# Performance work log

Measured on AMD Instinct MI355X. Metric: run time of the kernel, lower is better.

## Reference

```python
import jax, jax.numpy as jnp
import numpy as np

EMB = 300; TOWERS = 6; LAYERS = 4; EPS = 1e-5; F_OUT = EMB // TOWERS  # 50
N_NODES = 3000; N_EDGES = 9000; N_GRAPHS = 64
NODE_VOCAB = 16; EDGE_VOCAB = 4


def _bn(x, g, b, m, v):
    # eval-mode BatchNorm1d with running stats
    return (x - m) * jax.lax.rsqrt(v + EPS) * g + b


def _forward(node_emb, edge_emb, W_edge, b_edge, W_pre, b_pre, W_post, b_post,
             W_lin, b_lin, bn_gamma, bn_beta, bn_mean, bn_var,
             head_w0, head_b0, gn0_gamma, gn0_beta, gn0_mean, gn0_var,
             head_w1, head_b1, gn1_gamma, gn1_beta, gn1_mean, gn1_var,
             head_w2, head_b2, x, edge_index, edge_attr, batch, num_graphs):
    N = x.shape[0]
    src, dst = edge_index[0], edge_index[1]
    h = node_emb[x]            # [N, D] node encoder (categorical embedding)
    e = edge_emb[edge_attr]    # [E, D] edge encoder
    cnt = jax.ops.segment_sum(jnp.ones(src.shape, h.dtype), dst, num_segments=N)
    deg = jnp.maximum(cnt, 1.0)
    log_deg = jnp.log(deg + 1.0)
    avg_log = jnp.mean(jnp.log(cnt + 1.0))  # PNA avg_deg['log'] of degree histogram
    amp = (log_deg / avg_log)[:, None, None]
    att = (avg_log / log_deg)[:, None, None]
    has_nb = (cnt > 0)[:, None, None]
    degc = deg[:, None, None]

    h_list = [h]
    for l in range(LAYERS):
        eproj = e @ W_edge[l] + b_edge[l]                        # [E, D]
        hcat = jnp.concatenate([h[dst], h[src], eproj], -1)      # [E, 3D] = [x_i, x_j, e]
        m = jnp.einsum('ef,tfd->etd', hcat, W_pre[l]) + b_pre[l]  # [E, T, D] per-tower pre-MLP
        s = jax.ops.segment_sum(m, dst, num_segments=N)
        mean = s / degc
        mn = jnp.where(has_nb, jax.ops.segment_min(m, dst, num_segments=N), 0.0)
        mx = jnp.where(has_nb, jax.ops.segment_max(m, dst, num_segments=N), 0.0)
        var = jax.ops.segment_sum(m * m, dst, num_segments=N) / degc - mean * mean
        std = jnp.sqrt(jax.nn.relu(var) + EPS)
        agg = jnp.concatenate([mean, mn, mx, std], -1)           # [N, T, 4D]
        agg = jnp.concatenate([agg, agg * amp, agg * att], -1)   # [N, T, 12D] scalers
        x_rep = jnp.broadcast_to(h[:, None, :], (N, TOWERS, EMB))
        post_in = jnp.concatenate([x_rep, agg], -1)              # [N, T, 13D]
        out = jnp.einsum('ntf,tfo->nto', post_in, W_post[l]) + b_post[l]  # [N, T, F_OUT]
        out = out.reshape(N, EMB) @ W_lin[l] + b_lin[l]
        out = _bn(out, bn_gamma[l], bn_beta[l], bn_mean[l], bn_var[l])
        if l < LAYERS - 1:
            out = jax.nn.relu(out)  # dropout is identity in eval mode
        h_list.append(out)
        h = out
    # JK='sum' exactly as in the original forward: sums h_list[0..num_layer-1]
    node_rep = h_list[0]
    for l in range(1, LAYERS):
        node_rep = node_rep + h_list[l]
    g = jax.ops.segment_sum(node_rep, batch, num_segments=num_graphs)  # global_add_pool
    g = jax.nn.relu(_bn(g @ head_w0 + head_b0, gn0_gamma, gn0_beta, gn0_mean, gn0_var))
    g = jax.nn.relu(_bn(g @ head_w1 + head_b1, gn1_gamma, gn1_beta, gn1_mean, gn1_var))
    return g @ head_w2 + head_b2


def setup_inputs() -> dict:
    key = jax.random.key(0)
    ks = jax.random.split(key, 16)
    D, T, L = EMB, TOWERS, LAYERS
    def rn(k, shape, s=0.05):
        return jax.random.normal(k, shape, dtype=jnp.float32) * s
    return {
        'x': jax.random.randint(ks[0], (N_NODES,), 0, NODE_VOCAB, dtype=jnp.int32),
        'edge_index': jax.random.randint(ks[1], (2, N_EDGES), 0, N_NODES, dtype=jnp.int32),
        'edge_attr': jax.random.randint(ks[2], (N_EDGES,), 0, EDGE_VOCAB, dtype=jnp.int32),
        'batch': jnp.sort(jax.random.randint(ks[3], (N_NODES,), 0, N_GRAPHS, dtype=jnp.int32)),
        'num_graphs': N_GRAPHS,
        'node_emb': rn(ks[4], (NODE_VOCAB, D), 1.0),
        'edge_emb': rn(ks[5], (EDGE_VOCAB, D), 1.0),
        'W_edge': rn(ks[6], (L, D, D)), 'b_edge': jnp.zeros((L, D), jnp.float32),
        'W_pre': rn(ks[7], (L, T, 3 * D, D)), 'b_pre': jnp.zeros((L, T, D), jnp.float32),
        'W_post': rn(ks[8], (L, T, 13 * D, F_OUT)), 'b_post': jnp.zeros((L, T, F_OUT), jnp.float32),
        'W_lin': rn(ks[9], (L, D, D)), 'b_lin': jnp.zeros((L, D), jnp.float32),
        'bn_gamma': jnp.ones((L, D), jnp.float32), 'bn_beta': jnp.zeros((L, D), jnp.float32),
        'bn_mean': jnp.zeros((L, D), jnp.float32), 'bn_var': jnp.ones((L, D), jnp.float32),
        'head_w0': rn(ks[10], (D, 2 * D)), 'head_b0': jnp.zeros((2 * D,), jnp.float32),
        'gn0_gamma': jnp.ones((2 * D,), jnp.float32), 'gn0_beta': jnp.zeros((2 * D,), jnp.float32),
        'gn0_mean': jnp.zeros((2 * D,), jnp.float32), 'gn0_var': jnp.ones((2 * D,), jnp.float32),
        'head_w1': rn(ks[11], (2 * D, D)), 'head_b1': jnp.zeros((D,), jnp.float32),
        'gn1_gamma': jnp.ones((D,), jnp.float32), 'gn1_beta': jnp.zeros((D,), jnp.float32),
        'gn1_mean': jnp.zeros((D,), jnp.float32), 'gn1_var': jnp.ones((D,), jnp.float32),
        'head_w2': rn(ks[12], (D, 1)), 'head_b2': jnp.zeros((1,), jnp.float32),
    }


def reference(x, edge_index, edge_attr, batch, num_graphs,
              node_emb, edge_emb, W_edge, b_edge, W_pre, b_pre, W_post, b_post,
              W_lin, b_lin, bn_gamma, bn_beta, bn_mean, bn_var,
              head_w0, head_b0, gn0_gamma, gn0_beta, gn0_mean, gn0_var,
              head_w1, head_b1, gn1_gamma, gn1_beta, gn1_mean, gn1_var,
              head_w2, head_b2):
    return _forward(node_emb, edge_emb, W_edge, b_edge, W_pre, b_pre, W_post, b_post,
                    W_lin, b_lin, bn_gamma, bn_beta, bn_mean, bn_var,
                    head_w0, head_b0, gn0_gamma, gn0_beta, gn0_mean, gn0_var,
                    head_w1, head_b1, gn1_gamma, gn1_beta, gn1_mean, gn1_var,
                    head_w2, head_b2, x, edge_index, edge_attr, batch, num_graphs)
```

## Files before the change

kernel.cpp:

```cpp
#include <hip/hip_runtime.h>
#include <math.h>

#define NN 3000
#define NE 9000
#define NG 64
#define D 300
#define NT 6
#define FO 50
#define EPSV 1e-5f

__global__ void k_hist(const int* __restrict__ dst, int* __restrict__ cnt) {
    int e = blockIdx.x * blockDim.x + threadIdx.x;
    if (e < NE) atomicAdd(&cnt[dst[e]], 1);
}

__global__ __launch_bounds__(1024) void k_scan(
    const int* __restrict__ cnt, int* __restrict__ row_ptr, int* __restrict__ tmp_ptr,
    float* __restrict__ degf, float* __restrict__ ampv, float* __restrict__ attv) {
    __shared__ int s_part[1024];
    __shared__ float s_log[1024];
    int tid = threadIdx.x;
    int base = tid * 3;
    int c0 = 0, c1 = 0, c2 = 0; float lg = 0.f;
    if (base + 0 < NN) { c0 = cnt[base + 0]; lg += logf((float)c0 + 1.f); }
    if (base + 1 < NN) { c1 = cnt[base + 1]; lg += logf((float)c1 + 1.f); }
    if (base + 2 < NN) { c2 = cnt[base + 2]; lg += logf((float)c2 + 1.f); }
    s_part[tid] = c0 + c1 + c2;
    s_log[tid] = lg;
    __syncthreads();
    for (int off = 1; off < 1024; off <<= 1) {
        int v = (tid >= off) ? s_part[tid - off] : 0;
        __syncthreads();
        s_part[tid] += v;
        __syncthreads();
    }
    for (int off = 512; off > 0; off >>= 1) {
        if (tid < off) s_log[tid] += s_log[tid + off];
        __syncthreads();
    }
    float avg = s_log[0] / (float)NN;
    int run = (tid > 0) ? s_part[tid - 1] : 0;
    int cs[3] = {c0, c1, c2};
    for (int i = 0; i < 3; i++) {
        int n = base + i;
        if (n < NN) {
            row_ptr[n] = run; tmp_ptr[n] = run;
            int cc = cs[i];
            float dd = (float)(cc > 0 ? cc : 1);
            degf[n] = dd;
            float ld = logf(dd + 1.f);
            ampv[n] = ld / avg;
            attv[n] = avg / ld;
            run += cc;
        }
    }
    if (tid == 1023) row_ptr[NN] = s_part[1023];
}

__global__ void k_fill(const int* __restrict__ src, const int* __restrict__ dst,
                       const int* __restrict__ attr, int* __restrict__ tmp_ptr,
                       int2* __restrict__ edge_dat) {
    int e = blockIdx.x * blockDim.x + threadIdx.x;
    if (e < NE) {
        int d = dst[e];
        int p = atomicAdd(&tmp_ptr[d], 1);
        edge_dat[p] = make_int2(src[e], attr[e]);
    }
}

__global__ void k_embed(const int* __restrict__ x, const float* __restrict__ node_emb,
                        float* __restrict__ h, float* __restrict__ rep) {
    int i = blockIdx.x * blockDim.x + threadIdx.x;
    if (i < NN * D) {
        int n = i / D, d = i - n * D;
        float v = node_emb[x[n] * D + d];
        h[i] = v; rep[i] = v;
    }
}

__global__ void k_pack1(const float* __restrict__ W_pre, int l, float* __restrict__ Bp) {
    int idx = blockIdx.x * blockDim.x + threadIdx.x;
    if (idx >= 300 * 3600) return;
    int f = idx / 3600, j = idx - f * 3600;
    int s = j / 1800, r = j - s * 1800;
    int t = r / 300, d = r - t * 300;
    Bp[idx] = W_pre[(((size_t)(l * NT + t) * 900) + s * 300 + f) * 300 + d];
}

__global__ void k_packx(const float* __restrict__ W_post, int l, float* __restrict__ Bp) {
    int idx = blockIdx.x * blockDim.x + threadIdx.x;
    if (idx >= 300 * 300) return;
    int f = idx / 300, j = idx - f * 300;
    int t = j / FO, o = j - t * FO;
    Bp[idx] = W_post[((size_t)(l * NT + t) * 3900 + f) * FO + o];
}

__global__ void k_packpost(const float* __restrict__ W_post, int l, float* __restrict__ Bp) {
    int idx = blockIdx.x * blockDim.x + threadIdx.x;
    if (idx >= NT * 1200 * 160) return;
    int t = idx / 192000, r = idx - t * 192000;
    int f = r / 160, c = r - f * 160;
    float v = 0.f;
    if (c < 150) {
        int k = c / FO, o = c - k * FO;
        v = W_post[((size_t)(l * NT + t) * 3900 + 300 + k * 1200 + f) * FO + o];
    }
    Bp[idx] = v;
}

__global__ void k_ep4(const float* __restrict__ edge_emb, const float* __restrict__ W_edge,
                      const float* __restrict__ b_edge, int l, float* __restrict__ ep4) {
    int idx = blockIdx.x * blockDim.x + threadIdx.x;
    if (idx >= 4 * 300) return;
    int a = idx / 300, f = idx - a * 300;
    float s = b_edge[l * 300 + f];
    for (int k = 0; k < 300; k++)
        s = fmaf(edge_emb[a * 300 + k], W_edge[((size_t)l * 300 + k) * 300 + f], s);
    ep4[idx] = s;
}

__global__ void k_ep_proj(const float* __restrict__ ep4, const float* __restrict__ W_pre,
                          const float* __restrict__ b_pre, int l, float* __restrict__ Ep) {
    int idx = blockIdx.x * blockDim.x + threadIdx.x;
    if (idx >= 4 * 1800) return;
    int a = idx / 1800, c = idx - a * 1800;
    int t = c / 300, d = c - t * 300;
    float s = b_pre[(l * NT + t) * 300 + d];
    for (int f = 0; f < 300; f++)
        s = fmaf(ep4[a * 300 + f], W_pre[(((size_t)(l * NT + t) * 900) + 600 + f) * 300 + d], s);
    Ep[idx] = s;
}

__global__ void k_pack_lin(const float* __restrict__ W_lin, const float* __restrict__ b_lin,
                           const float* __restrict__ gam, const float* __restrict__ bet,
                           const float* __restrict__ mu, const float* __restrict__ var,
                           int l, float* __restrict__ Wf, float* __restrict__ bf) {
    int idx = blockIdx.x * blockDim.x + threadIdx.x;
    if (idx >= 300 * 300) return;
    int f = idx / 300, j = idx - f * 300;
    float s = gam[l * 300 + j] * rsqrtf(var[l * 300 + j] + EPSV);
    Wf[idx] = W_lin[((size_t)l * 300 + f) * 300 + j] * s;
    if (f == 0) bf[j] = (b_lin[l * 300 + j] - mu[l * 300 + j]) * s + bet[l * 300 + j];
}

template <int EPI>
__global__ __launch_bounds__(256) void k_gemm(
    const float* __restrict__ A, int lda, long long zA,
    const float* __restrict__ B, int ldb, long long zB,
    float* __restrict__ C, int ldc, long long zC,
    int M, int N, int K,
    const float* __restrict__ bias, float* __restrict__ rep) {
    constexpr int BM = 64, BN = 64, BK = 16, LAS = BM + 4;
    __shared__ float As[BK * LAS];
    __shared__ float Bs[BK * BN];
    A += (size_t)blockIdx.z * zA;
    B += (size_t)blockIdx.z * zB;
    C += (size_t)blockIdx.z * zC;
    int tid = threadIdx.x;
    int tx = tid & 15, ty = tid >> 4;
    int bm = blockIdx.y * BM, bn = blockIdx.x * BN;
    int arow = tid >> 2;
    int akq = (tid & 3) * 4;
    int bj = tid & 63, bk0 = tid >> 6;
    float acc[4][4] = {};
    for (int k0 = 0; k0 < K; k0 += BK) {
        {
            float4 av = make_float4(0.f, 0.f, 0.f, 0.f);
            int grow = bm + arow;
            if (grow < M) {
                int gk = k0 + akq;
                if (gk + 3 < K) {
                    av = *(const float4*)&A[(size_t)grow * lda + gk];
                } else {
                    float t0 = (gk + 0 < K) ? A[(size_t)grow * lda + gk + 0] : 0.f;
                    float t1 = (gk + 1 < K) ? A[(size_t)grow * lda + gk + 1] : 0.f;
                    float t2 = (gk + 2 < K) ? A[(size_t)grow * lda + gk + 2] : 0.f;
                    float t3 = (gk + 3 < K) ? A[(size_t)grow * lda + gk + 3] : 0.f;
                    av = make_float4(t0, t1, t2, t3);
                }
            }
            As[(akq + 0) * LAS + arow] = av.x;
            As[(akq + 1) * LAS + arow] = av.y;
            As[(akq + 2) * LAS + arow] = av.z;
            As[(akq + 3) * LAS + arow] = av.w;
        }
        #pragma unroll
        for (int it = 0; it < 4; ++it) {
            int k = bk0 + it * 4;
            int gk = k0 + k, gj = bn + bj;
            float v = 0.f;
            if (gk < K && gj < N) v = B[(size_t)gk * ldb + gj];
            Bs[k * BN + bj] = v;
        }
        __syncthreads();
        #pragma unroll
        for (int kk = 0; kk < BK; ++kk) {
            float4 a = *(const float4*)&As[kk * LAS + ty * 4];
            float4 b = *(const float4*)&Bs[kk * BN + tx * 4];
            float ar[4] = {a.x, a.y, a.z, a.w};
            float br[4] = {b.x, b.y, b.z, b.w};
            #pragma unroll
            for (int i = 0; i < 4; i++)
                #pragma unroll
                for (int j = 0; j < 4; j++)
                    acc[i][j] = fmaf(ar[i], br[j], acc[i][j]);
        }
        __syncthreads();
    }
    #pragma unroll
    for (int i = 0; i < 4; i++) {
        int r = bm + ty * 4 + i;
        if (r >= M) continue;
        #pragma unroll
        for (int j = 0; j < 4; j++) {
            int c = bn + tx * 4 + j;
            if (c >= N) continue;
            float v = acc[i][j];
            if (EPI == 1) {
                v += bias[c];
                v = fmaxf(v, 0.f);
                C[(size_t)r * ldc + c] = v;
                rep[(size_t)r * ldc + c] += v;
            } else {
                C[(size_t)r * ldc + c] = v;
            }
        }
    }
}

__global__ __launch_bounds__(256) void k_gemm1(const float* __restrict__ A,
                                               const float* __restrict__ B,
                                               float* __restrict__ C) {
    constexpr int BM = 128, BN = 128, BK = 16, LAS = BM + 4;
    constexpr int M = 3000, N = 3600, K = 300;
    __shared__ float As[BK * LAS];
    __shared__ float Bs[BK * BN];
    int tid = threadIdx.x;
    int tx = tid & 15, ty = tid >> 4;
    int bm = blockIdx.y * BM, bn = blockIdx.x * BN;
    float acc[8][8] = {};
    for (int k0 = 0; k0 < K; k0 += BK) {
        #pragma unroll
        for (int it = 0; it < 2; ++it) {
            int i = tid + it * 256;
            int row = i >> 2, kq = (i & 3) * 4;
            int grow = bm + row, gk = k0 + kq;
            float4 av = make_float4(0.f, 0.f, 0.f, 0.f);
            if (grow < M && gk < K) av = *(const float4*)&A[(size_t)grow * 300 + gk];
            As[(kq + 0) * LAS + row] = av.x;
            As[(kq + 1) * LAS + row] = av.y;
            As[(kq + 2) * LAS + row] = av.z;
            As[(kq + 3) * LAS + row] = av.w;
        }
        #pragma unroll
        for (int it = 0; it < 2; ++it) {
            int i = tid + it * 256;
            int k = i >> 5, c = (i & 31) * 4;
            int gk = k0 + k, gj = bn + c;
            float4 bv = make_float4(0.f, 0.f, 0.f, 0.f);
            if (gk < K && gj < N) bv = *(const float4*)&B[(size_t)gk * 3600 + gj];
            *(float4*)&Bs[k * BN + c] = bv;
        }
        __syncthreads();
        #pragma unroll
        for (int kk = 0; kk < BK; ++kk) {
            float a[8], b[8];
            *(float4*)&a[0] = *(const float4*)&As[kk * LAS + ty * 8];
            *(float4*)&a[4] = *(const float4*)&As[kk * LAS + ty * 8 + 4];
            *(float4*)&b[0] = *(const float4*)&Bs[kk * BN + tx * 8];
            *(float4*)&b[4] = *(const float4*)&Bs[kk * BN + tx * 8 + 4];
            #pragma unroll
            for (int i = 0; i < 8; i++)
                #pragma unroll
                for (int j = 0; j < 8; j++)
                    acc[i][j] = fmaf(a[i], b[j], acc[i][j]);
        }
        __syncthreads();
    }
    int r0 = bm + ty * 8, c0 = bn + tx * 8;
    #pragma unroll
    for (int i = 0; i < 8; i++) {
        int r = r0 + i;
        if (r >= M) break;
        if (c0 + 8 <= N) {
            float4 v0 = make_float4(acc[i][0], acc[i][1], acc[i][2], acc[i][3]);
            float4 v1 = make_float4(acc[i][4], acc[i][5], acc[i][6], acc[i][7]);
            *(float4*)&C[(size_t)r * 3600 + c0] = v0;
            *(float4*)&C[(size_t)r * 3600 + c0 + 4] = v1;
        } else {
            #pragma unroll
            for (int j = 0; j < 8; j++)
                if (c0 + j < N) C[(size_t)r * 3600 + c0 + j] = acc[i][j];
        }
    }
}

__global__ __launch_bounds__(256) void k_gemmp(const float* __restrict__ agg,
                                               const float* __restrict__ Bp,
                                               float* __restrict__ P) {
    constexpr int BM = 64, BN = 160, BK = 16, LAS = BM + 4, KC = 400;
    __shared__ float As[BK * LAS];
    __shared__ float Bs[BK * BN];
    int z = blockIdx.z;
    int t = z % 6, kc = z / 6;
    const float* A = agg + t * 1200 + kc * KC;
    const float* B = Bp + t * 192000 + kc * KC * 160;
    float* C = P + (size_t)z * 480000;
    int tid = threadIdx.x;
    int tx = tid & 15, ty = tid >> 4;
    int bm = blockIdx.y * BM;
    float acc[4][10] = {};
    for (int k0 = 0; k0 < KC; k0 += BK) {
        {
            int row = tid >> 2, kq = (tid & 3) * 4;
            int grow = bm + row;
            float4 av = make_float4(0.f, 0.f, 0.f, 0.f);
            if (grow < 3000) av = *(const float4*)&A[(size_t)grow * 7200 + k0 + kq];
            As[(kq + 0) * LAS + row] = av.x;
            As[(kq + 1) * LAS + row] = av.y;
            As[(kq + 2) * LAS + row] = av.z;
            As[(kq + 3) * LAS + row] = av.w;
        }
        #pragma unroll
        for (int it = 0; it < 3; ++it) {
            int i = tid + it * 256;
            if (i < 640) {
                int k = i / 40, c = (i - k * 40) * 4;
                *(float4*)&Bs[k * BN + c] = *(const float4*)&B[(size_t)(k0 + k) * 160 + c];
            }
        }
        __syncthreads();
        #pragma unroll
        for (int kk = 0; kk < BK; ++kk) {
            float a[4], b[10];
            *(float4*)&a[0] = *(const float4*)&As[kk * LAS + ty * 4];
            #pragma unroll
            for (int j = 0; j < 10; j++) b[j] = Bs[kk * BN + tx * 10 + j];
            #pragma unroll
            for (int i = 0; i < 4; i++)
                #pragma unroll
                for (int j = 0; j < 10; j++)
                    acc[i][j] = fmaf(a[i], b[j], acc[i][j]);
        }
        __syncthreads();
    }
    int r0 = bm + ty * 4, c0 = tx * 10;
    #pragma unroll
    for (int i = 0; i < 4; i++) {
        int r = r0 + i;
        if (r >= 3000) break;
        #pragma unroll
        for (int j = 0; j < 10; j++)
            C[(size_t)r * 160 + c0 + j] = acc[i][j];
    }
}

__global__ __launch_bounds__(256) void k_agg(
    const float* __restrict__ HH, const float* __restrict__ Ep,
    const int* __restrict__ row_ptr, const int2* __restrict__ edge_dat,
    const float* __restrict__ degf, const int* __restrict__ xv, int use_vocab,
    float* __restrict__ agg) {
    int n = blockIdx.x;
    int e0 = row_ptr[n], e1 = row_ptr[n + 1];
    int cnt = e1 - e0;
    float cntf = (float)cnt;
    float deg = degf[n];
    float inv_deg = 1.f / deg;
    int nrow = use_vocab ? xv[n] : n;
    const float* hdrow = HH + (size_t)nrow * 3600;
    for (int c4 = threadIdx.x; c4 < 450; c4 += 256) {
        int c = c4 * 4;
        float sx = 0.f, sy = 0.f, sz = 0.f, sw = 0.f;
        float qx = 0.f, qy = 0.f, qz = 0.f, qw = 0.f;
        float mnx = INFINITY, mny = INFINITY, mnz = INFINITY, mnw = INFINITY;
        float mxx = -INFINITY, mxy = -INFINITY, mxz = -INFINITY, mxw = -INFINITY;
        for (int e = e0; e < e1; ++e) {
            int2 sa = edge_dat[e];
            int srow = use_vocab ? xv[sa.x] : sa.x;
            float4 hv = *(const float4*)&HH[(size_t)srow * 3600 + 1800 + c];
            float4 ev = *(const float4*)&Ep[(size_t)sa.y * 1800 + c];
            float vx = hv.x + ev.x, vy = hv.y + ev.y, vz = hv.z + ev.z, vw = hv.w + ev.w;
            sx += vx; sy += vy; sz += vz; sw += vw;
            qx = fmaf(vx, vx, qx); qy = fmaf(vy, vy, qy);
            qz = fmaf(vz, vz, qz); qw = fmaf(vw, vw, qw);
            mnx = fminf(mnx, vx); mny = fminf(mny, vy);
            mnz = fminf(mnz, vz); mnw = fminf(mnw, vw);
            mxx = fmaxf(mxx, vx); mxy = fmaxf(mxy, vy);
            mxz = fmaxf(mxz, vz); mxw = fmaxf(mxw, vw);
        }
        float4 hd = *(const float4*)&hdrow[c];
        float4 mean, mnv, mxv, stdv;
        {
            mean.x = (cntf * hd.x + sx) * inv_deg;
            mean.y = (cntf * hd.y + sy) * inv_deg;
            mean.z = (cntf * hd.z + sz) * inv_deg;
            mean.w = (cntf * hd.w + sw) * inv_deg;
            if (cnt > 0) {
                mnv.x = hd.x + mnx; mnv.y = hd.y + mny; mnv.z = hd.z + mnz; mnv.w = hd.w + mnw;
                mxv.x = hd.x + mxx; mxv.y = hd.y + mxy; mxv.z = hd.z + mxz; mxv.w = hd.w + mxw;
            } else {
                mnv = make_float4(0.f, 0.f, 0.f, 0.f);
                mxv = make_float4(0.f, 0.f, 0.f, 0.f);
            }
            float vrx = (cntf * hd.x * hd.x + 2.f * hd.x * sx + qx) * inv_deg - mean.x * mean.x;
            float vry = (cntf * hd.y * hd.y + 2.f * hd.y * sy + qy) * inv_deg - mean.y * mean.y;
            float vrz = (cntf * hd.z * hd.z + 2.f * hd.z * sz + qz) * inv_deg - mean.z * mean.z;
            float vrw = (cntf * hd.w * hd.w + 2.f * hd.w * sw + qw) * inv_deg - mean.w * mean.w;
            stdv.x = sqrtf(fmaxf(vrx, 0.f) + EPSV);
            stdv.y = sqrtf(fmaxf(vry, 0.f) + EPSV);
            stdv.z = sqrtf(fmaxf(vrz, 0.f) + EPSV);
            stdv.w = sqrtf(fmaxf(vrw, 0.f) + EPSV);
        }
        int t = c / 300, d = c - t * 300;
        float* arow = agg + (size_t)n * 7200 + (size_t)t * 1200 + d;
        *(float4*)&arow[0]   = mean;
        *(float4*)&arow[300] = mnv;
        *(float4*)&arow[600] = mxv;
        *(float4*)&arow[900] = stdv;
    }
}

__global__ void k_combine(const float* __restrict__ Xp, const float* __restrict__ P,
                          const float* __restrict__ ampv, const float* __restrict__ attv,
                          const float* __restrict__ b_post_l, const int* __restrict__ xv,
                          int use_vocab, float* __restrict__ out_pre) {
    int i = blockIdx.x * blockDim.x + threadIdx.x;
    if (i >= NN * D) return;
    int n = i / D, j = i - n * D;
    int t = j / FO, o = j - t * FO;
    int nrow = use_vocab ? xv[n] : n;
    float p1 = 0.f, p2 = 0.f, p3 = 0.f;
    #pragma unroll
    for (int kc = 0; kc < 3; kc++) {
        const float* Pr = P + ((size_t)(kc * 6 + t) * 3000 + n) * 160;
        p1 += Pr[o];
        p2 += Pr[50 + o];
        p3 += Pr[100 + o];
    }
    float v = Xp[(size_t)nrow * D + j] + p1 + ampv[n] * p2 + attv[n] * p3
              + b_post_l[t * FO + o];
    out_pre[i] = v;
}

__global__ __launch_bounds__(256) void k_pool(const float* __restrict__ rep,
                                              const int* __restrict__ batch,
                                              float* __restrict__ g) {
    __shared__ int s_lo, s_hi;
    int b = blockIdx.x;
    if (threadIdx.x == 0) {
        int lo = 0, hi = NN;
        while (lo < hi) { int m = (lo + hi) >> 1; if (batch[m] < b) lo = m + 1; else hi = m; }
        s_lo = lo;
        int lo2 = lo, hi2 = NN;
        while (lo2 < hi2) { int m = (lo2 + hi2) >> 1; if (batch[m] < b + 1) lo2 = m + 1; else hi2 = m; }
        s_hi = lo2;
    }
    __syncthreads();
    int lo = s_lo, hi = s_hi;
    for (int j = threadIdx.x; j < D; j += blockDim.x) {
        float s = 0.f;
        for (int n = lo; n < hi; ++n) s += rep[(size_t)n * D + j];
        g[b * D + j] = s;
    }
}

__global__ __launch_bounds__(256) void k_head(const float* __restrict__ g,
                                              const float* __restrict__ W,
                                              const float* __restrict__ bh,
                                              const float* __restrict__ gam,
                                              const float* __restrict__ bet,
                                              const float* __restrict__ mu,
                                              const float* __restrict__ var,
                                              float* __restrict__ outg, int Kd, int Nd) {
    __shared__ float s_a[600];
    int b = blockIdx.x;
    for (int k = threadIdx.x; k < Kd; k += 256) s_a[k] = g[b * Kd + k];
    __syncthreads();
    for (int j = threadIdx.x; j < Nd; j += 256) {
        float s = 0.f;
        for (int k = 0; k < Kd; k++) s = fmaf(s_a[k], W[(size_t)k * Nd + j], s);
        s += bh[j];
        s = (s - mu[j]) * rsqrtf(var[j] + EPSV) * gam[j] + bet[j];
        s = fmaxf(s, 0.f);
        outg[b * Nd + j] = s;
    }
}

__global__ void k_head2(const float* __restrict__ g2, const float* __restrict__ w2,
                        const float* __restrict__ b2, float* __restrict__ out) {
    int b = blockIdx.x;
    int tid = threadIdx.x;
    float s = 0.f;
    for (int k = tid; k < 300; k += 64) s += g2[b * 300 + k] * w2[k];
    for (int off = 32; off; off >>= 1) s += __shfl_down(s, off, 64);
    if (tid == 0) out[b] = s + b2[0];
}

extern "C" void kernel_launch(void* const* d_in, const int* in_sizes, int n_in,
                              void* d_out, int out_size, void* d_ws, size_t ws_size,
                              hipStream_t stream) {
    const int* x      = (const int*)d_in[0];
    const int* ei     = (const int*)d_in[1];
    const int* src    = ei;
    const int* dst    = ei + NE;
    const int* eattr  = (const int*)d_in[2];
    const int* batch  = (const int*)d_in[3];
    const float* node_emb = (const float*)d_in[5];
    const float* edge_emb = (const float*)d_in[6];
    const float* W_edge   = (const float*)d_in[7];
    const float* b_edge   = (const float*)d_in[8];
    const float* W_pre    = (const float*)d_in[9];
    const float* b_pre    = (const float*)d_in[10];
    const float* W_post   = (const float*)d_in[11];
    const float* b_post   = (const float*)d_in[12];
    const float* W_lin    = (const float*)d_in[13];
    const float* b_lin    = (const float*)d_in[14];
    const float* bn_gamma = (const float*)d_in[15];
    const float* bn_beta  = (const float*)d_in[16];
    const float* bn_mean  = (const float*)d_in[17];
    const float* bn_var   = (const float*)d_in[18];
    const float* head_w0  = (const float*)d_in[19];
    const float* head_b0  = (const float*)d_in[20];
    const float* gn0_g    = (const float*)d_in[21];
    const float* gn0_b    = (const float*)d_in[22];
    const float* gn0_m    = (const float*)d_in[23];
    const float* gn0_v    = (const float*)d_in[24];
    const float* head_w1  = (const float*)d_in[25];
    const float* head_b1  = (const float*)d_in[26];
    const float* gn1_g    = (const float*)d_in[27];
    const float* gn1_b    = (const float*)d_in[28];
    const float* gn1_m    = (const float*)d_in[29];
    const float* gn1_v    = (const float*)d_in[30];
    const float* head_w2  = (const float*)d_in[31];
    const float* head_b2  = (const float*)d_in[32];
    float* out = (float*)d_out;

    unsigned char* base = (unsigned char*)d_ws;
    size_t off = 0;
    auto alloc = [&](size_t bytes) -> void* {
        void* p = base + off;
        off += (bytes + 255) & ~(size_t)255;
        return p;
    };
    int*   cnt      = (int*)alloc(NN * 4);
    int*   row_ptr  = (int*)alloc((NN + 1) * 4);
    int*   tmp_ptr  = (int*)alloc(NN * 4);
    int2*  edge_dat = (int2*)alloc(NE * 8);
    float* degf     = (float*)alloc(NN * 4);
    float* ampv     = (float*)alloc(NN * 4);
    float* attv     = (float*)alloc(NN * 4);
    float* h        = (float*)alloc((size_t)NN * D * 4);
    float* rep      = (float*)alloc((size_t)NN * D * 4);
    float* HsHd     = (float*)alloc((size_t)NN * 3600 * 4);
    float* Bpack1   = (float*)alloc((size_t)300 * 3600 * 4);
    float* ep4      = (float*)alloc(4 * 300 * 4);
    float* Ep       = (float*)alloc(4 * 1800 * 4);
    float* agg      = (float*)alloc((size_t)NN * 7200 * 4);
    float* Bpost    = (float*)alloc((size_t)NT * 1200 * 160 * 4);
    float* Wpx      = (float*)alloc((size_t)300 * 300 * 4);
    float* Xp       = (float*)alloc((size_t)NN * D * 4);
    float* P        = (float*)alloc((size_t)18 * 3000 * 160 * 4);
    float* out_pre  = (float*)alloc((size_t)NN * D * 4);
    float* Wlin_f   = (float*)alloc((size_t)300 * 300 * 4);
    float* b_f      = (float*)alloc(300 * 4);
    float* gsum     = (float*)alloc(NG * D * 4);
    float* gbuf0    = (float*)alloc(NG * 600 * 4);
    float* gbuf1    = (float*)alloc(NG * 300 * 4);
    (void)ws_size; (void)n_in; (void)in_sizes; (void)out_size;

    hipMemsetAsync(cnt, 0, NN * 4, stream);
    k_hist<<<(NE + 255) / 256, 256, 0, stream>>>(dst, cnt);
    k_scan<<<1, 1024, 0, stream>>>(cnt, row_ptr, tmp_ptr, degf, ampv, attv);
    k_fill<<<(NE + 255) / 256, 256, 0, stream>>>(src, dst, eattr, tmp_ptr, edge_dat);
    k_embed<<<(NN * D + 255) / 256, 256, 0, stream>>>(x, node_emb, h, rep);

    for (int l = 0; l < 3; ++l) {
        const float* Ain = (l == 0) ? node_emb : h;
        int M = (l == 0) ? 16 : NN;
        int uv = (l == 0) ? 1 : 0;

        k_pack1<<<(300 * 3600 + 255) / 256, 256, 0, stream>>>(W_pre, l, Bpack1);
        if (l == 0) {
            k_gemm<0><<<dim3(57, 1, 1), 256, 0, stream>>>(
                Ain, 300, 0, Bpack1, 3600, 0, HsHd, 3600, 0, M, 3600, 300, nullptr, nullptr);
        } else {
            k_gemm1<<<dim3(29, 24, 1), 256, 0, stream>>>(Ain, Bpack1, HsHd);
        }

        k_ep4<<<(1200 + 255) / 256, 256, 0, stream>>>(edge_emb, W_edge, b_edge, l, ep4);
        k_ep_proj<<<(7200 + 255) / 256, 256, 0, stream>>>(ep4, W_pre, b_pre, l, Ep);

        k_packx<<<(300 * 300 + 255) / 256, 256, 0, stream>>>(W_post, l, Wpx);
        k_gemm<0><<<dim3(5, (M + 63) / 64, 1), 256, 0, stream>>>(
            Ain, 300, 0, Wpx, 300, 0, Xp, 300, 0, M, 300, 300, nullptr, nullptr);

        k_agg<<<NN, 256, 0, stream>>>(HsHd, Ep, row_ptr, edge_dat, degf, x, uv, agg);

        k_packpost<<<(NT * 1200 * 160 + 255) / 256, 256, 0, stream>>>(W_post, l, Bpost);
        k_gemmp<<<dim3(1, 47, 18), 256, 0, stream>>>(agg, Bpost, P);

        k_combine<<<(NN * D + 255) / 256, 256, 0, stream>>>(
            Xp, P, ampv, attv, b_post + l * NT * FO, x, uv, out_pre);

        k_pack_lin<<<(300 * 300 + 255) / 256, 256, 0, stream>>>(
            W_lin, b_lin, bn_gamma, bn_beta, bn_mean, bn_var, l, Wlin_f, b_f);
        k_gemm<1><<<dim3(5, 47, 1), 256, 0, stream>>>(
            out_pre, 300, 0, Wlin_f, 300, 0, h, 300, 0, NN, 300, 300, b_f, rep);
    }

    k_pool<<<NG, 256, 0, stream>>>(rep, batch, gsum);
    k_head<<<NG, 256, 0, stream>>>(gsum, head_w0, head_b0, gn0_g, gn0_b, gn0_m, gn0_v,
                                   gbuf0, 300, 600);
    k_head<<<NG, 256, 0, stream>>>(gbuf0, head_w1, head_b1, gn1_g, gn1_b, gn1_m, gn1_v,
                                   gbuf1, 600, 300);
    k_head2<<<NG, 64, 0, stream>>>(gbuf1, head_w2, head_b2, out);
}
```

Measured before the change: 1.520 ms.

## Fuse root-term projection into main GEMM and run head MLP via tiled GEMM

The W_post root-node weight slice (x_i term) is packed as 300 extra columns alongside the W_pre projection, so one GEMM produces both the per-node pre-MLP projections and the post-MLP root projection. This removes the separate packx kernel and its GEMM, and k_combine reads the root term from the widened HsHd buffer. The head MLP layers now run through the tiled k_gemm with a new BN+ReLU epilogue instead of a per-graph scalar matvec kernel. The cost is a wider HsHd row stride (3900), which k_agg also reads.

```diff
diff --git a/kernel.cpp b/kernel.cpp
--- a/kernel.cpp
+++ b/kernel.cpp
@@ -8,6 +8,7 @@
 #define NT 6
 #define FO 50
 #define EPSV 1e-5f
+#define NB1 3900
 
 __global__ void k_hist(const int* __restrict__ dst, int* __restrict__ cnt) {
     int e = blockIdx.x * blockDim.x + threadIdx.x;
@@ -78,21 +79,22 @@
     }
 }
 
-__global__ void k_pack1(const float* __restrict__ W_pre, int l, float* __restrict__ Bp) {
+__global__ void k_pack1(const float* __restrict__ W_pre, const float* __restrict__ W_post,
+                        int l, float* __restrict__ Bp) {
     int idx = blockIdx.x * blockDim.x + threadIdx.x;
-    if (idx >= 300 * 3600) return;
-    int f = idx / 3600, j = idx - f * 3600;
-    int s = j / 1800, r = j - s * 1800;
-    int t = r / 300, d = r - t * 300;
-    Bp[idx] = W_pre[(((size_t)(l * NT + t) * 900) + s * 300 + f) * 300 + d];
-}
-
-__global__ void k_packx(const float* __restrict__ W_post, int l, float* __restrict__ Bp) {
-    int idx = blockIdx.x * blockDim.x + threadIdx.x;
-    if (idx >= 300 * 300) return;
-    int f = idx / 300, j = idx - f * 300;
-    int t = j / FO, o = j - t * FO;
-    Bp[idx] = W_post[((size_t)(l * NT + t) * 3900 + f) * FO + o];
+    if (idx >= 300 * NB1) return;
+    int f = idx / NB1, j = idx - f * NB1;
+    float v;
+    if (j < 3600) {
+        int s = j / 1800, r = j - s * 1800;
+        int t = r / 300, d = r - t * 300;
+        v = W_pre[(((size_t)(l * NT + t) * 900) + s * 300 + f) * 300 + d];
+    } else {
+        int jj = j - 3600;
+        int t = jj / FO, o = jj - t * FO;
+        v = W_post[((size_t)(l * NT + t) * 3900 + f) * FO + o];
+    }
+    Bp[idx] = v;
 }
 
 __global__ void k_packpost(const float* __restrict__ W_post, int l, float* __restrict__ Bp) {
@@ -145,17 +147,16 @@
 
 template <int EPI>
 __global__ __launch_bounds__(256) void k_gemm(
-    const float* __restrict__ A, int lda, long long zA,
-    const float* __restrict__ B, int ldb, long long zB,
-    float* __restrict__ C, int ldc, long long zC,
+    const float* __restrict__ A, int lda,
+    const float* __restrict__ B, int ldb,
+    float* __restrict__ C, int ldc,
     int M, int N, int K,
-    const float* __restrict__ bias, float* __restrict__ rep) {
+    const float* __restrict__ bias, float* __restrict__ rep,
+    const float* __restrict__ gam, const float* __restrict__ bet,
+    const float* __restrict__ mu, const float* __restrict__ var) {
     constexpr int BM = 64, BN = 64, BK = 16, LAS = BM + 4;
     __shared__ float As[BK * LAS];
     __shared__ float Bs[BK * BN];
-    A += (size_t)blockIdx.z * zA;
-    B += (size_t)blockIdx.z * zB;
-    C += (size_t)blockIdx.z * zC;
     int tid = threadIdx.x;
     int tx = tid & 15, ty = tid >> 4;
     int bm = blockIdx.y * BM, bn = blockIdx.x * BN;
@@ -221,6 +222,11 @@
                 v = fmaxf(v, 0.f);
                 C[(size_t)r * ldc + c] = v;
                 rep[(size_t)r * ldc + c] += v;
+            } else if (EPI == 2) {
+                v += bias[c];
+                v = (v - mu[c]) * rsqrtf(var[c] + EPSV) * gam[c] + bet[c];
+                v = fmaxf(v, 0.f);
+                C[(size_t)r * ldc + c] = v;
             } else {
                 C[(size_t)r * ldc + c] = v;
             }
@@ -232,7 +238,7 @@
                                                const float* __restrict__ B,
                                                float* __restrict__ C) {
     constexpr int BM = 128, BN = 128, BK = 16, LAS = BM + 4;
-    constexpr int M = 3000, N = 3600, K = 300;
+    constexpr int M = 3000, N = NB1, K = 300;
     __shared__ float As[BK * LAS];
     __shared__ float Bs[BK * BN];
     int tid = threadIdx.x;
@@ -258,7 +264,7 @@
             int k = i >> 5, c = (i & 31) * 4;
             int gk = k0 + k, gj = bn + c;
             float4 bv = make_float4(0.f, 0.f, 0.f, 0.f);
-            if (gk < K && gj < N) bv = *(const float4*)&B[(size_t)gk * 3600 + gj];
+            if (gk < K && gj < N) bv = *(const float4*)&B[(size_t)gk * N + gj];
             *(float4*)&Bs[k * BN + c] = bv;
         }
         __syncthreads();
@@ -285,12 +291,12 @@
         if (c0 + 8 <= N) {
             float4 v0 = make_float4(acc[i][0], acc[i][1], acc[i][2], acc[i][3]);
             float4 v1 = make_float4(acc[i][4], acc[i][5], acc[i][6], acc[i][7]);
-            *(float4*)&C[(size_t)r * 3600 + c0] = v0;
-            *(float4*)&C[(size_t)r * 3600 + c0 + 4] = v1;
+            *(float4*)&C[(size_t)r * N + c0] = v0;
+            *(float4*)&C[(size_t)r * N + c0 + 4] = v1;
         } else {
             #pragma unroll
             for (int j = 0; j < 8; j++)
-                if (c0 + j < N) C[(size_t)r * 3600 + c0 + j] = acc[i][j];
+                if (c0 + j < N) C[(size_t)r * N + c0 + j] = acc[i][j];
         }
     }
 }
@@ -367,7 +373,7 @@
     float deg = degf[n];
     float inv_deg = 1.f / deg;
     int nrow = use_vocab ? xv[n] : n;
-    const float* hdrow = HH + (size_t)nrow * 3600;
+    const float* hdrow = HH + (size_t)nrow * NB1;
     for (int c4 = threadIdx.x; c4 < 450; c4 += 256) {
         int c = c4 * 4;
         float sx = 0.f, sy = 0.f, sz = 0.f, sw = 0.f;
@@ -377,7 +383,7 @@
         for (int e = e0; e < e1; ++e) {
             int2 sa = edge_dat[e];
             int srow = use_vocab ? xv[sa.x] : sa.x;
-            float4 hv = *(const float4*)&HH[(size_t)srow * 3600 + 1800 + c];
+            float4 hv = *(const float4*)&HH[(size_t)srow * NB1 + 1800 + c];
             float4 ev = *(const float4*)&Ep[(size_t)sa.y * 1800 + c];
             float vx = hv.x + ev.x, vy = hv.y + ev.y, vz = hv.z + ev.z, vw = hv.w + ev.w;
             sx += vx; sy += vy; sz += vz; sw += vw;
@@ -420,7 +426,7 @@
     }
 }
 
-__global__ void k_combine(const float* __restrict__ Xp, const float* __restrict__ P,
+__global__ void k_combine(const float* __restrict__ HH, const float* __restrict__ P,
                           const float* __restrict__ ampv, const float* __restrict__ attv,
                           const float* __restrict__ b_post_l, const int* __restrict__ xv,
                           int use_vocab, float* __restrict__ out_pre) {
@@ -437,7 +443,7 @@
         p2 += Pr[50 + o];
         p3 += Pr[100 + o];
     }
-    float v = Xp[(size_t)nrow * D + j] + p1 + ampv[n] * p2 + attv[n] * p3
+    float v = HH[(size_t)nrow * NB1 + 3600 + j] + p1 + ampv[n] * p2 + attv[n] * p3
               + b_post_l[t * FO + o];
     out_pre[i] = v;
 }
@@ -461,28 +467,6 @@
         float s = 0.f;
         for (int n = lo; n < hi; ++n) s += rep[(size_t)n * D + j];
         g[b * D + j] = s;
-    }
-}
-
-__global__ __launch_bounds__(256) void k_head(const float* __restrict__ g,
-                                              const float* __restrict__ W,
-                                              const float* __restrict__ bh,
-                                              const float* __restrict__ gam,
-                                              const float* __restrict__ bet,
-                                              const float* __restrict__ mu,
-                                              const float* __restrict__ var,
-                                              float* __restrict__ outg, int Kd, int Nd) {
-    __shared__ float s_a[600];
-    int b = blockIdx.x;
-    for (int k = threadIdx.x; k < Kd; k += 256) s_a[k] = g[b * Kd + k];
-    __syncthreads();
-    for (int j = threadIdx.x; j < Nd; j += 256) {
-        float s = 0.f;
-        for (int k = 0; k < Kd; k++) s = fmaf(s_a[k], W[(size_t)k * Nd + j], s);
-        s += bh[j];
-        s = (s - mu[j]) * rsqrtf(var[j] + EPSV) * gam[j] + bet[j];
-        s = fmaxf(s, 0.f);
-        outg[b * Nd + j] = s;
     }
 }
 
@@ -551,14 +535,12 @@
     float* attv     = (float*)alloc(NN * 4);
     float* h        = (float*)alloc((size_t)NN * D * 4);
     float* rep      = (float*)alloc((size_t)NN * D * 4);
-    float* HsHd     = (float*)alloc((size_t)NN * 3600 * 4);
-    float* Bpack1   = (float*)alloc((size_t)300 * 3600 * 4);
+    float* HsHd     = (float*)alloc((size_t)NN * NB1 * 4);
+    float* Bpack1   = (float*)alloc((size_t)300 * NB1 * 4);
     float* ep4      = (float*)alloc(4 * 300 * 4);
     float* Ep       = (float*)alloc(4 * 1800 * 4);
     float* agg      = (float*)alloc((size_t)NN * 7200 * 4);
     float* Bpost    = (float*)alloc((size_t)NT * 1200 * 160 * 4);
-    float* Wpx      = (float*)alloc((size_t)300 * 300 * 4);
-    float* Xp       = (float*)alloc((size_t)NN * D * 4);
     float* P        = (float*)alloc((size_t)18 * 3000 * 160 * 4);
     float* out_pre  = (float*)alloc((size_t)NN * D * 4);
     float* Wlin_f   = (float*)alloc((size_t)300 * 300 * 4);
@@ -579,39 +561,39 @@
         int M = (l == 0) ? 16 : NN;
         int uv = (l == 0) ? 1 : 0;
 
-        k_pack1<<<(300 * 3600 + 255) / 256, 256, 0, stream>>>(W_pre, l, Bpack1);
+        k_pack1<<<(300 * NB1 + 255) / 256, 256, 0, stream>>>(W_pre, W_post, l, Bpack1);
         if (l == 0) {
-            k_gemm<0><<<dim3(57, 1, 1), 256, 0, stream>>>(
-                Ain, 300, 0, Bpack1, 3600, 0, HsHd, 3600, 0, M, 3600, 300, nullptr, nullptr);
+            k_gemm<0><<<dim3((NB1 + 63) / 64, 1, 1), 256, 0, stream>>>(
+                Ain, 300, Bpack1, NB1, HsHd, NB1, M, NB1, 300,
+                nullptr, nullptr, nullptr, nullptr, nullptr, nullptr);
         } else {
-            k_gemm1<<<dim3(29, 24, 1), 256, 0, stream>>>(Ain, Bpack1, HsHd);
+            k_gemm1<<<dim3((NB1 + 127) / 128, 24, 1), 256, 0, stream>>>(Ain, Bpack1, HsHd);
         }
 
         k_ep4<<<(1200 + 255) / 256, 256, 0, stream>>>(edge_emb, W_edge, b_edge, l, ep4);
         k_ep_proj<<<(7200 + 255) / 256, 256, 0, stream>>>(ep4, W_pre, b_pre, l, Ep);
 
-        k_packx<<<(300 * 300 + 255) / 256, 256, 0, stream>>>(W_post, l, Wpx);
-        k_gemm<0><<<dim3(5, (M + 63) / 64, 1), 256, 0, stream>>>(
-            Ain, 300, 0, Wpx, 300, 0, Xp, 300, 0, M, 300, 300, nullptr, nullptr);
-
         k_agg<<<NN, 256, 0, stream>>>(HsHd, Ep, row_ptr, edge_dat, degf, x, uv, agg);
 
         k_packpost<<<(NT * 1200 * 160 + 255) / 256, 256, 0, stream>>>(W_post, l, Bpost);
         k_gemmp<<<dim3(1, 47, 18), 256, 0, stream>>>(agg, Bpost, P);
 
         k_combine<<<(NN * D + 255) / 256, 256, 0, stream>>>(
-            Xp, P, ampv, attv, b_post + l * NT * FO, x, uv, out_pre);
+            HsHd, P, ampv, attv, b_post + l * NT * FO, x, uv, out_pre);
 
         k_pack_lin<<<(300 * 300 + 255) / 256, 256, 0, stream>>>(
             W_lin, b_lin, bn_gamma, bn_beta, bn_mean, bn_var, l, Wlin_f, b_f);
         k_gemm<1><<<dim3(5, 47, 1), 256, 0, stream>>>(
-            out_pre, 300, 0, Wlin_f, 300, 0, h, 300, 0, NN, 300, 300, b_f, rep);
+            out_pre, 300, Wlin_f, 300, h, 300, NN, 300, 300,
+            b_f, rep, nullptr, nullptr, nullptr, nullptr);
     }
 
     k_pool<<<NG, 256, 0, stream>>>(rep, batch, gsum);
-    k_head<<<NG, 256, 0, stream>>>(gsum, head_w0, head_b0, gn0_g, gn0_b, gn0_m, gn0_v,
-                                   gbuf0, 300, 600);
-    k_head<<<NG, 256, 0, stream>>>(gbuf0, head_w1, head_b1, gn1_g, gn1_b, gn1_m, gn1_v,
-                                   gbuf1, 600, 300);
+    k_gemm<2><<<dim3(10, 1, 1), 256, 0, stream>>>(
+        gsum, 300, head_w0, 600, gbuf0, 600, NG, 600, 300,
+        head_b0, nullptr, gn0_g, gn0_b, gn0_m, gn0_v);
+    k_gemm<2><<<dim3(5, 1, 1), 256, 0, stream>>>(
+        gbuf0, 600, head_w1, 300, gbuf1, 300, NG, 300, 600,
+        head_b1, nullptr, gn1_g, gn1_b, gn1_m, gn1_v);
     k_head2<<<NG, 64, 0, stream>>>(gbuf1, head_w2, head_b2, out);
 }
```

Result: faster. 1.317 ms (-13.3%).
